# Kernel tuning notes

Measured on AMD Instinct MI355X. Metric: run time of the kernel, lower is better.

Reference implementation:

```python
import jax, jax.numpy as jnp
import numpy as np

N_NODES = 100000
N_EDGES = 3200000
N_GRAPHS = 1024
HID = 64
NUM_CLASSES = 21


def setup_inputs() -> dict:
    key = jax.random.key(0)
    ks = jax.random.split(key, 12)
    x = jax.random.normal(ks[0], (N_NODES, 1), dtype=jnp.float32)
    edge_index = jax.random.randint(ks[1], (2, N_EDGES), 0, N_NODES, dtype=jnp.int64)
    batch = jnp.sort(jax.random.randint(ks[2], (N_NODES,), 0, N_GRAPHS, dtype=jnp.int64))
    def lin(k, fan_in, fan_out):
        bound = 1.0 / np.sqrt(fan_in)
        return jax.random.uniform(k, (fan_in, fan_out), jnp.float32, -bound, bound)
    return {
        "x": x,
        "edge_index": edge_index,
        "batch": batch,
        # SAGEConv1: lin_l (on aggregated neighbors, with bias), lin_r (root, no bias)
        "W1l": lin(ks[3], 1, HID), "b1": jnp.zeros((HID,), jnp.float32), "W1r": lin(ks[4], 1, HID),
        # SAGEConv2
        "W2l": lin(ks[5], HID, HID), "b2": jnp.zeros((HID,), jnp.float32), "W2r": lin(ks[6], HID, HID),
        # classifier
        "Wc": lin(ks[7], HID, NUM_CLASSES), "bc": jnp.zeros((NUM_CLASSES,), jnp.float32),
    }


def _sage_conv(x, src, dst, Wl, bl, Wr):
    # mean-aggregate neighbor features: gather from src, scatter-mean to dst
    msg = x[src]                                              # [E, F] gather
    agg = jax.ops.segment_sum(msg, dst, num_segments=N_NODES)  # [N, F]
    cnt = jax.ops.segment_sum(jnp.ones((src.shape[0],), x.dtype), dst, num_segments=N_NODES)
    agg = agg / jnp.maximum(cnt, 1.0)[:, None]
    # out = lin_l(aggr) + lin_r(x)
    return agg @ Wl + bl + x @ Wr


def reference(x, edge_index, batch, W1l, b1, W1r, W2l, b2, W2r, Wc, bc):
    src, dst = edge_index[0], edge_index[1]
    h = jax.nn.relu(_sage_conv(x, src, dst, W1l, b1, W1r))
    h = jax.nn.relu(_sage_conv(h, src, dst, W2l, b2, W2r))
    # global mean pool over graphs
    pooled = jax.ops.segment_sum(h, batch, num_segments=N_GRAPHS)
    gcnt = jax.ops.segment_sum(jnp.ones((h.shape[0],), h.dtype), batch, num_segments=N_GRAPHS)
    pooled = pooled / jnp.maximum(gcnt, 1.0)[:, None]
    return pooled @ Wc + bc
```

## Files before the change

kernel.cpp:

```cpp
#include <hip/hip_runtime.h>

#define N_NODES 100000
#define N_EDGES 3200000
#define N_GRAPHS 1024
#define NCLS 21
#define NBKT 782
#define CAP 4480
#define NB 512
#define CHUNK 6250
#define TROW 72

typedef short s8v __attribute__((ext_vector_type(8)));
typedef float f4v __attribute__((ext_vector_type(4)));

__device__ __forceinline__ float bf2f(unsigned short u) {
    return __uint_as_float(((unsigned)u) << 16);
}
__device__ __forceinline__ unsigned short f2bf(float f) {
    unsigned u = __float_as_uint(f);
    unsigned r = 0x7fffu + ((u >> 16) & 1u);
    return (unsigned short)((u + r) >> 16);
}
__device__ __forceinline__ float lo2f(unsigned w) { return __uint_as_float(w << 16); }
__device__ __forceinline__ float hi2f(unsigned w) { return __uint_as_float(w & 0xffff0000u); }

__global__ void k_prep(const float* __restrict__ W2l, const float* __restrict__ W2r,
                       unsigned short* __restrict__ wp,
                       const int* __restrict__ batch, int* __restrict__ gstart,
                       int* __restrict__ gcur) {
    if (blockIdx.x < 32) {
        int tid = blockIdx.x * 256 + threadIdx.x;
        int frag = tid >> 9;
        int r = tid & 511;
        int L = r >> 3, j = r & 7;
        int kstep = frag >> 2, nt = frag & 3;
        int k = kstep * 32 + (L >> 4) * 8 + j;
        int n = nt * 16 + (L & 15);
        float val = (k < 64) ? W2l[k * 64 + n] : W2r[(k - 64) * 64 + n];
        wp[tid] = f2bf(val);
    } else if (blockIdx.x < 37) {
        int g = (blockIdx.x - 32) * 256 + threadIdx.x;
        if (g > N_GRAPHS) return;
        if (g == N_GRAPHS) { gstart[N_GRAPHS] = N_NODES; return; }
        int lo = 0, hi = N_NODES;
        while (lo < hi) { int m = (lo + hi) >> 1; if (batch[m] < g) lo = m + 1; else hi = m; }
        gstart[g] = lo;
    } else {
        for (int i = threadIdx.x; i < NBKT; i += 256) gcur[i] = i * CAP;
    }
}

__global__ __launch_bounds__(256) void k_binone(const int* __restrict__ src,
                                                const int* __restrict__ dst,
                                                int* __restrict__ gcur,
                                                unsigned int* __restrict__ bins) {
    __shared__ unsigned int ebuf[CHUNK];
    __shared__ unsigned short bbuf[CHUNK];
    __shared__ int lh[NBKT];
    __shared__ int lbase[NBKT];
    int t = threadIdx.x;
    for (int i = t; i < NBKT; i += 256) lh[i] = 0;
    __syncthreads();
    const int2* s2 = (const int2*)(src + blockIdx.x * CHUNK);
    const int2* d2 = (const int2*)(dst + blockIdx.x * CHUNK);
    for (int i = t; i < CHUNK / 2; i += 256) {
        int2 s = s2[i];
        int2 d = d2[i];
        uint2 pp;
        pp.x = ((unsigned)s.x << 7) | (unsigned)(d.x & 127);
        pp.y = ((unsigned)s.y << 7) | (unsigned)(d.y & 127);
        *(uint2*)(&ebuf[2 * i]) = pp;
        bbuf[2 * i]     = (unsigned short)(d.x >> 7);
        bbuf[2 * i + 1] = (unsigned short)(d.y >> 7);
        atomicAdd(&lh[d.x >> 7], 1);
        atomicAdd(&lh[d.y >> 7], 1);
    }
    __syncthreads();
    for (int i = t; i < NBKT; i += 256)
        lbase[i] = atomicAdd(&gcur[i], lh[i]);
    __syncthreads();
    for (int i = t; i < NBKT; i += 256) lh[i] = lbase[i];
    __syncthreads();
    for (int i = t; i < CHUNK; i += 256) {
        int b = (int)bbuf[i];
        int pos = atomicAdd(&lh[b], 1);
        if (pos < (b + 1) * CAP) bins[pos] = ebuf[i];
    }
}

__global__ __launch_bounds__(256) void k_build(
    const int* __restrict__ gcur, unsigned int* __restrict__ bins,
    int* __restrict__ row, unsigned short* __restrict__ deg,
    const float* __restrict__ x,
    const float* __restrict__ W1l, const float* __restrict__ b1,
    const float* __restrict__ W1r, unsigned short* __restrict__ h1b) {
    __shared__ unsigned int ebuf[CAP];
    __shared__ int hist[128];
    __shared__ int curs[128];
    __shared__ int lds[128];
    __shared__ float t1[128];
    int k = blockIdx.x, t = threadIdx.x;
    int e0 = k * CAP;
    int cnt = min(gcur[k] - e0, CAP);
    if (t < 128) { hist[t] = 0; t1[t] = 0.0f; }
    __syncthreads();
    for (int i = t; i < cnt; i += 256) {
        unsigned p = bins[e0 + i];
        ebuf[i] = p;
        atomicAdd(&hist[p & 127u], 1);
    }
    __syncthreads();
    if (t < 128) lds[t] = hist[t];
    __syncthreads();
    for (int off = 1; off < 128; off <<= 1) {
        int cur = (t < 128) ? lds[t] : 0;
        int add = (t < 128 && t >= off) ? lds[t - off] : 0;
        __syncthreads();
        if (t < 128) lds[t] = cur + add;
        __syncthreads();
    }
    if (t < 128) {
        int run = e0 + lds[t] - hist[t];
        curs[t] = run;
        int n = k * 128 + t;
        if (n < N_NODES) { row[n] = run; deg[n] = (unsigned short)hist[t]; }
    }
    __syncthreads();
    for (int i = t; i < cnt; i += 256) {
        unsigned p = ebuf[i];
        int slot = (int)(p & 127u);
        int pos = atomicAdd(&curs[slot], 1);
        bins[pos] = p >> 7;
        atomicAdd(&t1[slot], x[p >> 7]);
    }
    __syncthreads();
    for (int i = t; i < 128 * 64; i += 256) {
        int slot = i >> 6, f = i & 63;
        int n = k * 128 + slot;
        if (n >= N_NODES) break;
        float a = t1[slot] / fmaxf((float)hist[slot], 1.0f);
        float v = a * W1l[f] + b1[f] + x[n] * W1r[f];
        h1b[(size_t)n * 64 + f] = f2bf(fmaxf(v, 0.0f));
    }
}

__global__ __launch_bounds__(256) void k_l2f(
    const int* __restrict__ row, const unsigned short* __restrict__ deg,
    const unsigned int* __restrict__ csr,
    const unsigned short* __restrict__ h1b,
    const unsigned short* __restrict__ wp, const float* __restrict__ b2,
    unsigned short* __restrict__ h2b) {
    __shared__ unsigned short tile[4][16 * TROW];
    int wid = threadIdx.x >> 6;
    int w = blockIdx.x * 4 + wid;
    if (w >= N_NODES / 16) return;
    int L = threadIdx.x & 63;
    int fo = L & 7;
    int es = L >> 3;
    int fown = fo * 8 + es;
    unsigned short* tw = tile[wid];

    for (int t = 0; t < 16; t++) {
        int n = w * 16 + t;
        int r0 = row[n];
        int dn = (int)deg[n];
        int r1 = r0 + dn;
        float a0 = 0.f, a1 = 0.f, a2 = 0.f, a3 = 0.f,
              a4 = 0.f, a5 = 0.f, a6 = 0.f, a7 = 0.f;
        int base = r0;
        for (; base + 32 <= r1; base += 32) {
            int sA = (int)csr[base + es];
            int sB = (int)csr[base + 8 + es];
            int sC = (int)csr[base + 16 + es];
            int sD = (int)csr[base + 24 + es];
            uint4 dA = *(const uint4*)(h1b + (size_t)sA * 64 + fo * 8);
            uint4 dB = *(const uint4*)(h1b + (size_t)sB * 64 + fo * 8);
            uint4 dC = *(const uint4*)(h1b + (size_t)sC * 64 + fo * 8);
            uint4 dD = *(const uint4*)(h1b + (size_t)sD * 64 + fo * 8);
            a0 += lo2f(dA.x); a1 += hi2f(dA.x); a2 += lo2f(dA.y); a3 += hi2f(dA.y);
            a4 += lo2f(dA.z); a5 += hi2f(dA.z); a6 += lo2f(dA.w); a7 += hi2f(dA.w);
            a0 += lo2f(dB.x); a1 += hi2f(dB.x); a2 += lo2f(dB.y); a3 += hi2f(dB.y);
            a4 += lo2f(dB.z); a5 += hi2f(dB.z); a6 += lo2f(dB.w); a7 += hi2f(dB.w);
            a0 += lo2f(dC.x); a1 += hi2f(dC.x); a2 += lo2f(dC.y); a3 += hi2f(dC.y);
            a4 += lo2f(dC.z); a5 += hi2f(dC.z); a6 += lo2f(dC.w); a7 += hi2f(dC.w);
            a0 += lo2f(dD.x); a1 += hi2f(dD.x); a2 += lo2f(dD.y); a3 += hi2f(dD.y);
            a4 += lo2f(dD.z); a5 += hi2f(dD.z); a6 += lo2f(dD.w); a7 += hi2f(dD.w);
        }
        for (; base + 16 <= r1; base += 16) {
            int sA = (int)csr[base + es];
            int sB = (int)csr[base + 8 + es];
            uint4 dA = *(const uint4*)(h1b + (size_t)sA * 64 + fo * 8);
            uint4 dB = *(const uint4*)(h1b + (size_t)sB * 64 + fo * 8);
            a0 += lo2f(dA.x); a1 += hi2f(dA.x); a2 += lo2f(dA.y); a3 += hi2f(dA.y);
            a4 += lo2f(dA.z); a5 += hi2f(dA.z); a6 += lo2f(dA.w); a7 += hi2f(dA.w);
            a0 += lo2f(dB.x); a1 += hi2f(dB.x); a2 += lo2f(dB.y); a3 += hi2f(dB.y);
            a4 += lo2f(dB.z); a5 += hi2f(dB.z); a6 += lo2f(dB.w); a7 += hi2f(dB.w);
        }
        for (; base < r1; base += 8) {
            int e = base + es;
            bool act = e < r1;
            int sA = (int)csr[act ? e : r1 - 1];
            uint4 d = *(const uint4*)(h1b + (size_t)sA * 64 + fo * 8);
            unsigned m = act ? 0xffffffffu : 0u;
            d.x &= m; d.y &= m; d.z &= m; d.w &= m;
            a0 += lo2f(d.x); a1 += hi2f(d.x); a2 += lo2f(d.y); a3 += hi2f(d.y);
            a4 += lo2f(d.z); a5 += hi2f(d.z); a6 += lo2f(d.w); a7 += hi2f(d.w);
        }
        {
            bool hi = (es & 4) != 0;
            float s0 = hi ? a0 : a4, s1 = hi ? a1 : a5, s2 = hi ? a2 : a6, s3 = hi ? a3 : a7;
            float r0v = __shfl_xor(s0, 32, 64);
            float r1v = __shfl_xor(s1, 32, 64);
            float r2v = __shfl_xor(s2, 32, 64);
            float r3v = __shfl_xor(s3, 32, 64);
            a0 = (hi ? a4 : a0) + r0v;
            a1 = (hi ? a5 : a1) + r1v;
            a2 = (hi ? a6 : a2) + r2v;
            a3 = (hi ? a7 : a3) + r3v;
        }
        {
            bool hi = (es & 2) != 0;
            float s0 = hi ? a0 : a2, s1 = hi ? a1 : a3;
            float r0v = __shfl_xor(s0, 16, 64);
            float r1v = __shfl_xor(s1, 16, 64);
            a0 = (hi ? a2 : a0) + r0v;
            a1 = (hi ? a3 : a1) + r1v;
        }
        {
            bool hi = (es & 1) != 0;
            float s0 = hi ? a0 : a1;
            float r0v = __shfl_xor(s0, 8, 64);
            a0 = (hi ? a1 : a0) + r0v;
        }
        float inv = 1.0f / fmaxf((float)dn, 1.0f);
        tw[t * TROW + fown] = f2bf(a0 * inv);
    }

    int m = L & 15, q = L >> 4;
    int nrow = w * 16 + m;

    const s8v a0 = *(const s8v*)(tw + m * TROW + q * 8);
    const s8v a1 = *(const s8v*)(tw + m * TROW + 32 + q * 8);
    const s8v a2 = *(const s8v*)(h1b + (size_t)nrow * 64 + q * 8);
    const s8v a3 = *(const s8v*)(h1b + (size_t)nrow * 64 + 32 + q * 8);

#define LOADB(i) s8v B##i = *(const s8v*)(wp + (i) * 512 + L * 8)
    LOADB(0); LOADB(1); LOADB(2); LOADB(3);
    LOADB(4); LOADB(5); LOADB(6); LOADB(7);
    LOADB(8); LOADB(9); LOADB(10); LOADB(11);
    LOADB(12); LOADB(13); LOADB(14); LOADB(15);
#undef LOADB

    f4v acc0 = {0.f, 0.f, 0.f, 0.f}, acc1 = acc0, acc2 = acc0, acc3 = acc0;
    acc0 = __builtin_amdgcn_mfma_f32_16x16x32_bf16(a0, B0,  acc0, 0, 0, 0);
    acc0 = __builtin_amdgcn_mfma_f32_16x16x32_bf16(a1, B4,  acc0, 0, 0, 0);
    acc0 = __builtin_amdgcn_mfma_f32_16x16x32_bf16(a2, B8,  acc0, 0, 0, 0);
    acc0 = __builtin_amdgcn_mfma_f32_16x16x32_bf16(a3, B12, acc0, 0, 0, 0);
    acc1 = __builtin_amdgcn_mfma_f32_16x16x32_bf16(a0, B1,  acc1, 0, 0, 0);
    acc1 = __builtin_amdgcn_mfma_f32_16x16x32_bf16(a1, B5,  acc1, 0, 0, 0);
    acc1 = __builtin_amdgcn_mfma_f32_16x16x32_bf16(a2, B9,  acc1, 0, 0, 0);
    acc1 = __builtin_amdgcn_mfma_f32_16x16x32_bf16(a3, B13, acc1, 0, 0, 0);
    acc2 = __builtin_amdgcn_mfma_f32_16x16x32_bf16(a0, B2,  acc2, 0, 0, 0);
    acc2 = __builtin_amdgcn_mfma_f32_16x16x32_bf16(a1, B6,  acc2, 0, 0, 0);
    acc2 = __builtin_amdgcn_mfma_f32_16x16x32_bf16(a2, B10, acc2, 0, 0, 0);
    acc2 = __builtin_amdgcn_mfma_f32_16x16x32_bf16(a3, B14, acc2, 0, 0, 0);
    acc3 = __builtin_amdgcn_mfma_f32_16x16x32_bf16(a0, B3,  acc3, 0, 0, 0);
    acc3 = __builtin_amdgcn_mfma_f32_16x16x32_bf16(a1, B7,  acc3, 0, 0, 0);
    acc3 = __builtin_amdgcn_mfma_f32_16x16x32_bf16(a2, B11, acc3, 0, 0, 0);
    acc3 = __builtin_amdgcn_mfma_f32_16x16x32_bf16(a3, B15, acc3, 0, 0, 0);

    int fcol = L & 15;
    float bia0 = b2[fcol], bia1 = b2[16 + fcol], bia2 = b2[32 + fcol], bia3 = b2[48 + fcol];
    int rbase = w * 16 + q * 4;
#pragma unroll
    for (int r = 0; r < 4; r++) {
        size_t o = (size_t)(rbase + r) * 64 + fcol;
        h2b[o]      = f2bf(fmaxf(acc0[r] + bia0, 0.0f));
        h2b[o + 16] = f2bf(fmaxf(acc1[r] + bia1, 0.0f));
        h2b[o + 32] = f2bf(fmaxf(acc2[r] + bia2, 0.0f));
        h2b[o + 48] = f2bf(fmaxf(acc3[r] + bia3, 0.0f));
    }
}

__global__ __launch_bounds__(256) void k_head(
    const unsigned short* __restrict__ h2b, const int* __restrict__ gstart,
    const float* __restrict__ Wc, const float* __restrict__ bc,
    float* __restrict__ out) {
    __shared__ float part[4][64];
    __shared__ float rowv[64];
    int g = blockIdx.x;
    int wid = threadIdx.x >> 6;
    int f = threadIdx.x & 63;
    int ns = gstart[g], ne = gstart[g + 1];
    float s = 0.0f;
    int n = ns + wid;
    for (; n + 12 < ne; n += 16) {
        float v0 = bf2f(h2b[(size_t)(n)      * 64 + f]);
        float v1 = bf2f(h2b[(size_t)(n + 4)  * 64 + f]);
        float v2 = bf2f(h2b[(size_t)(n + 8)  * 64 + f]);
        float v3 = bf2f(h2b[(size_t)(n + 12) * 64 + f]);
        s += (v0 + v1) + (v2 + v3);
    }
    for (; n < ne; n += 4) s += bf2f(h2b[(size_t)n * 64 + f]);
    part[wid][f] = s;
    __syncthreads();
    if (threadIdx.x < 64) {
        float tot = part[0][f] + part[1][f] + part[2][f] + part[3][f];
        rowv[f] = tot / fmaxf((float)(ne - ns), 1.0f);
    }
    __syncthreads();
    if (threadIdx.x < NCLS) {
        float acc = bc[threadIdx.x];
#pragma unroll
        for (int kk = 0; kk < 64; kk++) acc += rowv[kk] * Wc[kk * NCLS + threadIdx.x];
        out[g * NCLS + threadIdx.x] = acc;
    }
}

extern "C" void kernel_launch(void* const* d_in, const int* in_sizes, int n_in,
                              void* d_out, int out_size, void* d_ws, size_t ws_size,
                              hipStream_t stream) {
    const float* x     = (const float*)d_in[0];
    const int*   eidx  = (const int*)d_in[1];
    const int*   batch = (const int*)d_in[2];
    const float* W1l   = (const float*)d_in[3];
    const float* b1    = (const float*)d_in[4];
    const float* W1r   = (const float*)d_in[5];
    const float* W2l   = (const float*)d_in[6];
    const float* b2    = (const float*)d_in[7];
    const float* W2r   = (const float*)d_in[8];
    const float* Wc    = (const float*)d_in[9];
    const float* bc    = (const float*)d_in[10];
    float* out = (float*)d_out;

    const int* src = eidx;
    const int* dst = eidx + N_EDGES;

    char* p = (char*)d_ws;
    unsigned int* bins  = (unsigned int*)p;     p += (size_t)NBKT * CAP * 4;
    unsigned short* h1b = (unsigned short*)p;   p += (size_t)N_NODES * 64 * 2;
    unsigned short* h2b = (unsigned short*)p;   p += (size_t)N_NODES * 64 * 2;
    int* row   = (int*)p;                       p += (size_t)(N_NODES + 1) * 4;
    unsigned short* deg = (unsigned short*)p;   p += (size_t)N_NODES * 2;
    int* gcur  = (int*)p;                       p += NBKT * 4;
    int* gstart= (int*)p;                       p += (N_GRAPHS + 1) * 4;
    unsigned short* wp = (unsigned short*)p;    p += 8192 * 2;

    k_prep  <<<38, 256, 0, stream>>>(W2l, W2r, wp, batch, gstart, gcur);
    k_binone<<<NB, 256, 0, stream>>>(src, dst, gcur, bins);
    k_build <<<NBKT, 256, 0, stream>>>(gcur, bins, row, deg, x, W1l, b1, W1r, h1b);
    k_l2f   <<<(N_NODES / 16 + 3) / 4, 256, 0, stream>>>(row, deg, bins, h1b, wp, b2, h2b);
    k_head  <<<N_GRAPHS, 256, 0, stream>>>(h2b, gstart, Wc, bc, out);
}
```

Measured before the change: 228.5 us.

## Replace LDS edge staging with two-pass binning using per-wave histograms

The binning kernel no longer stages packed edges and bucket ids in shared memory. It counts with per-wave privatized histograms in a first pass, then re-reads src/dst from global memory and scatters directly, using two split cursors per bucket to reduce LDS atomic contention. This frees about 37KB of LDS per block, which may allow more resident blocks. The cost is a second global read of the dst array.

```diff
diff --git a/kernel.cpp b/kernel.cpp
--- a/kernel.cpp
+++ b/kernel.cpp
@@ -54,37 +54,41 @@
                                                 const int* __restrict__ dst,
                                                 int* __restrict__ gcur,
                                                 unsigned int* __restrict__ bins) {
-    __shared__ unsigned int ebuf[CHUNK];
-    __shared__ unsigned short bbuf[CHUNK];
-    __shared__ int lh[NBKT];
-    __shared__ int lbase[NBKT];
+    __shared__ int lh[4][NBKT];
+    __shared__ int lcur[2][NBKT];
     int t = threadIdx.x;
-    for (int i = t; i < NBKT; i += 256) lh[i] = 0;
+    int wid = t >> 6;
+    for (int i = t; i < 4 * NBKT; i += 256) ((int*)lh)[i] = 0;
+    __syncthreads();
+    const int2* d2 = (const int2*)(dst + blockIdx.x * CHUNK);
+    for (int i = t; i < CHUNK / 2; i += 256) {
+        int2 d = d2[i];
+        atomicAdd(&lh[wid][d.x >> 7], 1);
+        atomicAdd(&lh[wid][d.y >> 7], 1);
+    }
+    __syncthreads();
+    for (int i = t; i < NBKT; i += 256) {
+        int c0 = lh[0][i], c1 = lh[1][i], c2 = lh[2][i], c3 = lh[3][i];
+        int p0 = c0 + c1;
+        int tot = p0 + c2 + c3;
+        int base = atomicAdd(&gcur[i], tot);
+        lcur[0][i] = base;
+        lcur[1][i] = base + p0;
+    }
     __syncthreads();
     const int2* s2 = (const int2*)(src + blockIdx.x * CHUNK);
-    const int2* d2 = (const int2*)(dst + blockIdx.x * CHUNK);
+    int half = wid >> 1;
     for (int i = t; i < CHUNK / 2; i += 256) {
         int2 s = s2[i];
         int2 d = d2[i];
-        uint2 pp;
-        pp.x = ((unsigned)s.x << 7) | (unsigned)(d.x & 127);
-        pp.y = ((unsigned)s.y << 7) | (unsigned)(d.y & 127);
-        *(uint2*)(&ebuf[2 * i]) = pp;
-        bbuf[2 * i]     = (unsigned short)(d.x >> 7);
-        bbuf[2 * i + 1] = (unsigned short)(d.y >> 7);
-        atomicAdd(&lh[d.x >> 7], 1);
-        atomicAdd(&lh[d.y >> 7], 1);
-    }
-    __syncthreads();
-    for (int i = t; i < NBKT; i += 256)
-        lbase[i] = atomicAdd(&gcur[i], lh[i]);
-    __syncthreads();
-    for (int i = t; i < NBKT; i += 256) lh[i] = lbase[i];
-    __syncthreads();
-    for (int i = t; i < CHUNK; i += 256) {
-        int b = (int)bbuf[i];
-        int pos = atomicAdd(&lh[b], 1);
-        if (pos < (b + 1) * CAP) bins[pos] = ebuf[i];
+        int b0 = d.x >> 7;
+        int p0 = atomicAdd(&lcur[half][b0], 1);
+        if (p0 < (b0 + 1) * CAP)
+            bins[p0] = ((unsigned)s.x << 7) | (unsigned)(d.x & 127);
+        int b1 = d.y >> 7;
+        int p1 = atomicAdd(&lcur[half][b1], 1);
+        if (p1 < (b1 + 1) * CAP)
+            bins[p1] = ((unsigned)s.y << 7) | (unsigned)(d.y & 127);
     }
 }
 
```

Measured after the change: 241.8 us. +5.8%, slower.
